# Kernel tuning notes

Hardware: AMD Instinct MI355X
Metric: run time of the kernel (lower is better)

The kernel has to match this reference:

```python
import jax, jax.numpy as jnp
import numpy as np

N = 100_000      # nodes
E = 3_200_000    # edges (avg degree 32)
D_IN = 128
D_H = 128
EPS = 1e-12      # F.normalize eps


def setup_inputs() -> dict:
    key = jax.random.key(0)
    k1, k2, k3 = jax.random.split(key, 3)
    X = jax.random.normal(k1, (N, D_IN), dtype=jnp.float32)
    edge_index = jax.random.randint(k2, (2, E), 0, N, dtype=jnp.int32)
    # GCNConv linear weight (stored as [in, out] for X @ W) and bias
    W = jax.random.normal(k3, (D_IN, D_H), dtype=jnp.float32) / np.sqrt(D_IN)
    b = jnp.zeros((D_H,), dtype=jnp.float32)
    # MessageNorm learnable scale, init 1.0
    scale = jnp.ones((1,), dtype=jnp.float32)
    return {"X": X, "edge_index": edge_index, "W": W, "b": b, "scale": scale}


def reference(X, edge_index, W, b, scale):
    n = X.shape[0]
    loop = jnp.arange(n, dtype=edge_index.dtype)
    src = jnp.concatenate([edge_index[0], loop])  # add self loops
    tgt = jnp.concatenate([edge_index[1], loop])
    # symmetric GCN normalization: D^{-1/2} (A+I) D^{-1/2}
    deg = jax.ops.segment_sum(jnp.ones_like(src, X.dtype), tgt, num_segments=n)
    dinv = jnp.where(deg > 0, jax.lax.rsqrt(deg), 0.0)
    norm = dinv[src] * dinv[tgt]  # [E+N]
    XW = X @ W  # [N, D_H]
    msg = jax.ops.segment_sum(norm[:, None] * XW[src], tgt, num_segments=n) + b
    # MessageNorm(learn_scale=True): l2-normalize msg, rescale by ||x||_2 * scale
    msg_n = msg / jnp.maximum(jnp.linalg.norm(msg, axis=-1, keepdims=True), EPS)
    x_norm = jnp.linalg.norm(X, axis=-1, keepdims=True)
    return jax.nn.gelu(msg_n * x_norm * scale, approximate=False)
```

## Files before the change

kernel.cpp:

```cpp
#include <hip/hip_runtime.h>
#include <math.h>

#define D 128
#define NB 391
#define BSH 8
#define BMASK 255
#define CAP 10240
#define EPB 4096
#define LDA 136

typedef unsigned short ushort_t;
typedef unsigned int uint_t;
typedef __attribute__((ext_vector_type(8))) short bfrag;
typedef __attribute__((ext_vector_type(4))) float ffrag;

__device__ inline ushort_t f2bf(float f) {
    uint_t u = __float_as_uint(f);
    uint_t r = (u + 0x7FFFu + ((u >> 16) & 1u)) >> 16;
    return (ushort_t)r;
}

__global__ __launch_bounds__(256) void k_bin(const int* __restrict__ src,
                                             const int* __restrict__ tgt, int e,
                                             int* __restrict__ bucket_cur,
                                             uint_t* __restrict__ binned,
                                             const float* __restrict__ W,
                                             ushort_t* __restrict__ Wt) {
    __shared__ int lcnt[NB];
    __shared__ int lbase[NB];
    int tid = threadIdx.x;

    if (blockIdx.x < 16) {
        int nrow = blockIdx.x * 8 + (tid >> 5);
        int k0 = (tid & 31) * 4;
        ushort4 o;
        o.x = f2bf(W[(size_t)(k0 + 0) * D + nrow]);
        o.y = f2bf(W[(size_t)(k0 + 1) * D + nrow]);
        o.z = f2bf(W[(size_t)(k0 + 2) * D + nrow]);
        o.w = f2bf(W[(size_t)(k0 + 3) * D + nrow]);
        *(ushort4*)&Wt[(size_t)nrow * D + k0] = o;
    }

    int base = blockIdx.x * EPB;
    for (int i = tid; i < NB; i += 256) lcnt[i] = 0;
    __syncthreads();

    int myb[16], myrank[16];
    uint_t myval[16];
#pragma unroll
    for (int k = 0; k < 16; ++k) {
        int i = base + k * 256 + tid;
        if (i < e) {
            int t = tgt[i];
            int s = src[i];
            int b = t >> BSH;
            myb[k] = b;
            myval[k] = ((uint_t)s << BSH) | (uint_t)(t & BMASK);
            myrank[k] = atomicAdd(&lcnt[b], 1);
        } else {
            myb[k] = -1;
        }
    }
    __syncthreads();
    for (int i = tid; i < NB; i += 256) {
        int c = lcnt[i];
        lbase[i] = (c > 0) ? atomicAdd(&bucket_cur[i], c) : 0;
    }
    __syncthreads();
#pragma unroll
    for (int k = 0; k < 16; ++k) {
        if (myb[k] >= 0) {
            int slot = lbase[myb[k]] + myrank[k];
            if (slot < CAP) binned[(size_t)myb[k] * CAP + slot] = myval[k];
        }
    }
}

__global__ __launch_bounds__(256) void k_sort(const uint_t* __restrict__ binned,
                                              const int* __restrict__ bucket_cur,
                                              int* __restrict__ col,
                                              int* __restrict__ rowptr,
                                              float* __restrict__ dinv, int n) {
    __shared__ uint_t sout[CAP];
    __shared__ int scnt[256];
    __shared__ int sincl[256];
    __shared__ int sofs[256];
    __shared__ int sred[256];
    int b = blockIdx.x;
    int tid = threadIdx.x;

    int v = 0;
    for (int i = tid; i < b; i += 256) v += min(bucket_cur[i], CAP);
    sred[tid] = v;
    __syncthreads();
    for (int off = 128; off >= 1; off >>= 1) {
        if (tid < off) sred[tid] += sred[tid + off];
        __syncthreads();
    }
    int baseg = sred[0];

    int nb = min(bucket_cur[b], CAP);
    const uint_t* bin = binned + (size_t)b * CAP;

    scnt[tid] = 0;
    __syncthreads();
    for (int i = tid; i < nb; i += 256)
        atomicAdd(&scnt[bin[i] & BMASK], 1);
    __syncthreads();
    int x = scnt[tid];
    sincl[tid] = x;
    __syncthreads();
    for (int off = 1; off < 256; off <<= 1) {
        int y = (tid >= off) ? sincl[tid - off] : 0;
        __syncthreads();
        x += y;
        sincl[tid] = x;
        __syncthreads();
    }
    sofs[tid] = x - scnt[tid];
    int t = (b << BSH) + tid;
    if (t < n) {
        rowptr[t + 1] = baseg + x;
        dinv[t] = rsqrtf((float)scnt[tid] + 1.0f);
    }
    if (b == 0 && tid == 0) rowptr[0] = 0;
    __syncthreads();
    for (int i = tid; i < nb; i += 256) {
        uint_t w = bin[i];
        int r = atomicAdd(&sofs[w & BMASK], 1);
        sout[r] = w >> BSH;
    }
    __syncthreads();
    for (int i = tid; i < nb; i += 256)
        col[baseg + i] = (int)sout[i];
}

__global__ __launch_bounds__(256) void k_gemm(const float* __restrict__ X,
                                              const ushort_t* __restrict__ Wt,
                                              const float* __restrict__ dinv,
                                              ushort_t* __restrict__ Y,
                                              float* __restrict__ xnorm, int n) {
    __shared__ ushort_t As[64 * LDA];
    __shared__ ushort_t Bs[128 * LDA];
    int tid = threadIdx.x;
    int row0 = blockIdx.x * 64;

    for (int i = tid; i < 128 * 16; i += 256) {
        int nr = i >> 4, c = (i & 15) << 3;
        *(uint4*)&Bs[nr * LDA + c] = *(const uint4*)&Wt[(size_t)nr * D + c];
    }

    const float4* X4 = (const float4*)X;
#pragma unroll
    for (int i2 = 0; i2 < 8; ++i2) {
        int item = i2 * 256 + tid;
        int r = item >> 5, c4 = item & 31;
        int gr = row0 + r;
        float4 v = (gr < n) ? X4[(size_t)gr * 32 + c4] : make_float4(0.f, 0.f, 0.f, 0.f);
        ushort4 bv;
        bv.x = f2bf(v.x); bv.y = f2bf(v.y); bv.z = f2bf(v.z); bv.w = f2bf(v.w);
        *(ushort4*)&As[r * LDA + c4 * 4] = bv;
        float s = v.x * v.x + v.y * v.y + v.z * v.z + v.w * v.w;
        s += __shfl_xor(s, 1);
        s += __shfl_xor(s, 2);
        s += __shfl_xor(s, 4);
        s += __shfl_xor(s, 8);
        s += __shfl_xor(s, 16);
        if ((tid & 31) == 0 && gr < n) xnorm[gr] = sqrtf(s);
    }
    __syncthreads();

    int w = tid >> 6;
    int lane = tid & 63;
    int q = lane >> 4;
    int mi = lane & 15;

    bfrag xf[4];
#pragma unroll
    for (int kt = 0; kt < 4; ++kt)
        xf[kt] = *(const bfrag*)&As[(w * 16 + mi) * LDA + kt * 32 + q * 8];

    ffrag acc[8];
#pragma unroll
    for (int nt = 0; nt < 8; ++nt) acc[nt] = (ffrag){0.f, 0.f, 0.f, 0.f};

#pragma unroll
    for (int nt = 0; nt < 8; ++nt) {
#pragma unroll
        for (int kt = 0; kt < 4; ++kt) {
            bfrag wf = *(const bfrag*)&Bs[(nt * 16 + mi) * LDA + kt * 32 + q * 8];
            acc[nt] = __builtin_amdgcn_mfma_f32_16x16x32_bf16(wf, xf[kt], acc[nt], 0, 0, 0);
        }
    }

    int gr = row0 + w * 16 + mi;
    if (gr < n) {
        float dv = dinv[gr];
#pragma unroll
        for (int nt = 0; nt < 8; ++nt) {
            ushort4 o;
            o.x = f2bf(acc[nt][0] * dv);
            o.y = f2bf(acc[nt][1] * dv);
            o.z = f2bf(acc[nt][2] * dv);
            o.w = f2bf(acc[nt][3] * dv);
            *(ushort4*)&Y[(size_t)gr * D + nt * 16 + q * 4] = o;
        }
    }
}

__global__ __launch_bounds__(256) void k_agg(const ushort_t* __restrict__ Y,
                                             const float* __restrict__ xnorm,
                                             const float* __restrict__ dinv,
                                             const int* __restrict__ rowptr,
                                             const int* __restrict__ col,
                                             const float* __restrict__ bias,
                                             const float* __restrict__ scale,
                                             float* __restrict__ out, int n) {
    int t = (blockIdx.x * 256 + threadIdx.x) >> 6;
    int lane = threadIdx.x & 63;
    if (t >= n) return;

    const char* Yb = (const char*)Y;
    uint_t lo4 = (uint_t)lane * 4;

    uint_t p = *(const uint_t*)(Yb + (((uint_t)t << 8) + lo4));
    float a0 = __uint_as_float(p << 16);
    float a1 = __uint_as_float(p & 0xFFFF0000u);

    int beg = rowptr[t];
    int end = rowptr[t + 1];
    int e = beg;
    for (; e + 16 <= end; e += 16) {
        uint_t qv[16];
#pragma unroll
        for (int k = 0; k < 16; ++k) {
            int s = col[e + k];
            qv[k] = *(const uint_t*)(Yb + (((uint_t)s << 8) + lo4));
        }
#pragma unroll
        for (int k = 0; k < 16; ++k) {
            a0 += __uint_as_float(qv[k] << 16);
            a1 += __uint_as_float(qv[k] & 0xFFFF0000u);
        }
    }
    for (; e + 4 <= end; e += 4) {
        uint_t qv[4];
#pragma unroll
        for (int k = 0; k < 4; ++k) {
            int s = col[e + k];
            qv[k] = *(const uint_t*)(Yb + (((uint_t)s << 8) + lo4));
        }
#pragma unroll
        for (int k = 0; k < 4; ++k) {
            a0 += __uint_as_float(qv[k] << 16);
            a1 += __uint_as_float(qv[k] & 0xFFFF0000u);
        }
    }
    for (; e < end; ++e) {
        int s = col[e];
        uint_t q = *(const uint_t*)(Yb + (((uint_t)s << 8) + lo4));
        a0 += __uint_as_float(q << 16);
        a1 += __uint_as_float(q & 0xFFFF0000u);
    }

    float dt = dinv[t];
    float m0 = fmaf(dt, a0, bias[lane * 2]);
    float m1 = fmaf(dt, a1, bias[lane * 2 + 1]);

    float m2 = m0 * m0 + m1 * m1;
#pragma unroll
    for (int m = 32; m >= 1; m >>= 1) m2 += __shfl_xor(m2, m);

    float denom = fmaxf(sqrtf(m2), 1e-12f);
    float fac = xnorm[t] * scale[0] / denom;
    float g0 = m0 * fac;
    float g1 = m1 * fac;
    float2 o;
    o.x = 0.5f * g0 * (1.0f + erff(g0 * 0.70710678118654752440f));
    o.y = 0.5f * g1 * (1.0f + erff(g1 * 0.70710678118654752440f));
    *(float2*)&out[(size_t)t * D + lane * 2] = o;
}


extern "C" void kernel_launch(void* const* d_in, const int* in_sizes, int n_in,
                              void* d_out, int out_size, void* d_ws, size_t ws_size,
                              hipStream_t stream) {
    const float* X     = (const float*)d_in[0];
    const int*   ei    = (const int*)d_in[1];
    const float* W     = (const float*)d_in[2];
    const float* bias  = (const float*)d_in[3];
    const float* scale = (const float*)d_in[4];
    float* out = (float*)d_out;

    int n = in_sizes[0] / D;
    int e = in_sizes[1] / 2;
    const int* src = ei;
    const int* tgt = ei + e;

    char* ws = (char*)d_ws;
    ushort_t* Y = (ushort_t*)ws;   ws += (size_t)n * D * sizeof(ushort_t);
    uint_t* binned = (uint_t*)Y;
    float* dinv = (float*)ws;      ws += (size_t)n * sizeof(float);
    float* xnorm = (float*)ws;     ws += (size_t)n * sizeof(float);
    int* rowptr = (int*)ws;        ws += (size_t)(n + 1) * sizeof(int);
    int* bucket_cur = (int*)ws;    ws += NB * sizeof(int);
    int* col = (int*)ws;           ws += (size_t)e * sizeof(int);
    ushort_t* Wt = (ushort_t*)ws;

    hipMemsetAsync(bucket_cur, 0, NB * sizeof(int), stream);
    k_bin<<<(e + EPB - 1) / EPB, 256, 0, stream>>>(src, tgt, e, bucket_cur, binned, W, Wt);
    k_sort<<<NB, 256, 0, stream>>>(binned, bucket_cur, col, rowptr, dinv, n);
    k_gemm<<<(n + 63) / 64, 256, 0, stream>>>(X, Wt, dinv, Y, xnorm, n);
    k_agg<<<(n + 3) / 4, 256, 0, stream>>>(Y, xnorm, dinv, rowptr, col, bias, scale, out, n);
}
```

Before: 315.1 us.

## Replace bucketed bin-sort CSR build with degree count, scan, and atomic scatter

Replaces the two-pass bucket-binning and per-bucket shared-memory sort with a classic CSR build: global atomic degree histogram, a three-kernel prefix scan, then a per-edge atomic scatter into col. This removes the intermediate binned buffer and the CAP truncation limit, but relies on millions of global atomics to random addresses and adds extra kernel launches. The neighbour order inside each row becomes nondeterministic and no longer sorted, which may hurt locality in the aggregation gathers.

Result: slower. 670.4 us (+112.8%).

```diff
diff --git a/kernel.cpp b/kernel.cpp
--- a/kernel.cpp
+++ b/kernel.cpp
@@ -2,12 +2,8 @@
 #include <math.h>
 
 #define D 128
-#define NB 391
-#define BSH 8
-#define BMASK 255
-#define CAP 10240
-#define EPB 4096
 #define LDA 136
+#define EPT_BLK 2048
 
 typedef unsigned short ushort_t;
 typedef unsigned int uint_t;
@@ -20,14 +16,10 @@
     return (ushort_t)r;
 }
 
-__global__ __launch_bounds__(256) void k_bin(const int* __restrict__ src,
-                                             const int* __restrict__ tgt, int e,
-                                             int* __restrict__ bucket_cur,
-                                             uint_t* __restrict__ binned,
+__global__ __launch_bounds__(256) void k_deg(const int* __restrict__ tgt, int e,
+                                             int* __restrict__ deg,
                                              const float* __restrict__ W,
                                              ushort_t* __restrict__ Wt) {
-    __shared__ int lcnt[NB];
-    __shared__ int lbase[NB];
     int tid = threadIdx.x;
 
     if (blockIdx.x < 16) {
@@ -41,98 +33,87 @@
         *(ushort4*)&Wt[(size_t)nrow * D + k0] = o;
     }
 
-    int base = blockIdx.x * EPB;
-    for (int i = tid; i < NB; i += 256) lcnt[i] = 0;
+    int base = blockIdx.x * EPT_BLK;
+#pragma unroll
+    for (int k = 0; k < 8; ++k) {
+        int i = base + k * 256 + tid;
+        if (i < e) atomicAdd(&deg[tgt[i]], 1);
+    }
+}
+
+__global__ __launch_bounds__(256) void k_scan1(const int* __restrict__ deg,
+                                               int* __restrict__ rowptr,
+                                               float* __restrict__ dinv,
+                                               int* __restrict__ bsum, int n) {
+    __shared__ int s[256];
+    int tid = threadIdx.x;
+    int i = blockIdx.x * 256 + tid;
+    int d = (i < n) ? deg[i] : 0;
+    int x = d;
+    s[tid] = x;
     __syncthreads();
-
-    int myb[16], myrank[16];
-    uint_t myval[16];
-#pragma unroll
-    for (int k = 0; k < 16; ++k) {
+    for (int off = 1; off < 256; off <<= 1) {
+        int y = (tid >= off) ? s[tid - off] : 0;
+        __syncthreads();
+        x += y;
+        s[tid] = x;
+        __syncthreads();
+    }
+    if (i < n) {
+        rowptr[i + 1] = x;
+        dinv[i] = rsqrtf((float)d + 1.0f);
+    }
+    if (tid == 255) bsum[blockIdx.x] = x;
+}
+
+__global__ __launch_bounds__(512) void k_scan2(int* __restrict__ bsum, int nb) {
+    __shared__ int s[512];
+    int tid = threadIdx.x;
+    int v = (tid < nb) ? bsum[tid] : 0;
+    int x = v;
+    s[tid] = x;
+    __syncthreads();
+    for (int off = 1; off < 512; off <<= 1) {
+        int y = (tid >= off) ? s[tid - off] : 0;
+        __syncthreads();
+        x += y;
+        s[tid] = x;
+        __syncthreads();
+    }
+    if (tid < nb) bsum[tid] = x - v;
+}
+
+__global__ __launch_bounds__(256) void k_scan3(const int* __restrict__ deg,
+                                               int* __restrict__ rowptr,
+                                               int* __restrict__ cur,
+                                               const int* __restrict__ bsum, int n) {
+    int tid = threadIdx.x;
+    int i = blockIdx.x * 256 + tid;
+    int off = bsum[blockIdx.x];
+    if (i < n) {
+        int v = rowptr[i + 1] + off;
+        rowptr[i + 1] = v;
+        cur[i] = v - deg[i];
+    }
+    if (i == 0) rowptr[0] = 0;
+}
+
+__global__ __launch_bounds__(256) void k_scatter(const int* __restrict__ src,
+                                                 const int* __restrict__ tgt, int e,
+                                                 int* __restrict__ cur,
+                                                 int* __restrict__ col) {
+    int tid = threadIdx.x;
+    int base = blockIdx.x * EPT_BLK;
+#pragma unroll
+    for (int k = 0; k < 8; ++k) {
         int i = base + k * 256 + tid;
         if (i < e) {
             int t = tgt[i];
             int s = src[i];
-            int b = t >> BSH;
-            myb[k] = b;
-            myval[k] = ((uint_t)s << BSH) | (uint_t)(t & BMASK);
-            myrank[k] = atomicAdd(&lcnt[b], 1);
-        } else {
-            myb[k] = -1;
-        }
-    }
-    __syncthreads();
-    for (int i = tid; i < NB; i += 256) {
-        int c = lcnt[i];
-        lbase[i] = (c > 0) ? atomicAdd(&bucket_cur[i], c) : 0;
-    }
-    __syncthreads();
-#pragma unroll
-    for (int k = 0; k < 16; ++k) {
-        if (myb[k] >= 0) {
-            int slot = lbase[myb[k]] + myrank[k];
-            if (slot < CAP) binned[(size_t)myb[k] * CAP + slot] = myval[k];
-        }
-    }
-}
-
-__global__ __launch_bounds__(256) void k_sort(const uint_t* __restrict__ binned,
-                                              const int* __restrict__ bucket_cur,
-                                              int* __restrict__ col,
-                                              int* __restrict__ rowptr,
-                                              float* __restrict__ dinv, int n) {
-    __shared__ uint_t sout[CAP];
-    __shared__ int scnt[256];
-    __shared__ int sincl[256];
-    __shared__ int sofs[256];
-    __shared__ int sred[256];
-    int b = blockIdx.x;
-    int tid = threadIdx.x;
-
-    int v = 0;
-    for (int i = tid; i < b; i += 256) v += min(bucket_cur[i], CAP);
-    sred[tid] = v;
-    __syncthreads();
-    for (int off = 128; off >= 1; off >>= 1) {
-        if (tid < off) sred[tid] += sred[tid + off];
-        __syncthreads();
-    }
-    int baseg = sred[0];
-
-    int nb = min(bucket_cur[b], CAP);
-    const uint_t* bin = binned + (size_t)b * CAP;
-
-    scnt[tid] = 0;
-    __syncthreads();
-    for (int i = tid; i < nb; i += 256)
-        atomicAdd(&scnt[bin[i] & BMASK], 1);
-    __syncthreads();
-    int x = scnt[tid];
-    sincl[tid] = x;
-    __syncthreads();
-    for (int off = 1; off < 256; off <<= 1) {
-        int y = (tid >= off) ? sincl[tid - off] : 0;
-        __syncthreads();
-        x += y;
-        sincl[tid] = x;
-        __syncthreads();
-    }
-    sofs[tid] = x - scnt[tid];
-    int t = (b << BSH) + tid;
-    if (t < n) {
-        rowptr[t + 1] = baseg + x;
-        dinv[t] = rsqrtf((float)scnt[tid] + 1.0f);
-    }
-    if (b == 0 && tid == 0) rowptr[0] = 0;
-    __syncthreads();
-    for (int i = tid; i < nb; i += 256) {
-        uint_t w = bin[i];
-        int r = atomicAdd(&sofs[w & BMASK], 1);
-        sout[r] = w >> BSH;
-    }
-    __syncthreads();
-    for (int i = tid; i < nb; i += 256)
-        col[baseg + i] = (int)sout[i];
+            int p = atomicAdd(&cur[t], 1);
+            col[p] = s;
+        }
+    }
 }
 
 __global__ __launch_bounds__(256) void k_gemm(const float* __restrict__ X,
@@ -299,17 +280,24 @@
 
     char* ws = (char*)d_ws;
     ushort_t* Y = (ushort_t*)ws;   ws += (size_t)n * D * sizeof(ushort_t);
-    uint_t* binned = (uint_t*)Y;
     float* dinv = (float*)ws;      ws += (size_t)n * sizeof(float);
     float* xnorm = (float*)ws;     ws += (size_t)n * sizeof(float);
     int* rowptr = (int*)ws;        ws += (size_t)(n + 1) * sizeof(int);
-    int* bucket_cur = (int*)ws;    ws += NB * sizeof(int);
+    int* deg = (int*)ws;           ws += (size_t)n * sizeof(int);
+    int* cur = (int*)ws;           ws += (size_t)n * sizeof(int);
+    int* bsum = (int*)ws;          ws += 512 * sizeof(int);
     int* col = (int*)ws;           ws += (size_t)e * sizeof(int);
     ushort_t* Wt = (ushort_t*)ws;
 
-    hipMemsetAsync(bucket_cur, 0, NB * sizeof(int), stream);
-    k_bin<<<(e + EPB - 1) / EPB, 256, 0, stream>>>(src, tgt, e, bucket_cur, binned, W, Wt);
-    k_sort<<<NB, 256, 0, stream>>>(binned, bucket_cur, col, rowptr, dinv, n);
+    int nscan = (n + 255) / 256;
+    int nedge = (e + EPT_BLK - 1) / EPT_BLK;
+
+    hipMemsetAsync(deg, 0, (size_t)n * sizeof(int), stream);
+    k_deg<<<nedge, 256, 0, stream>>>(tgt, e, deg, W, Wt);
+    k_scan1<<<nscan, 256, 0, stream>>>(deg, rowptr, dinv, bsum, n);
+    k_scan2<<<1, 512, 0, stream>>>(bsum, nscan);
+    k_scan3<<<nscan, 256, 0, stream>>>(deg, rowptr, cur, bsum, n);
+    k_scatter<<<nedge, 256, 0, stream>>>(src, tgt, e, cur, col);
     k_gemm<<<(n + 63) / 64, 256, 0, stream>>>(X, Wt, dinv, Y, xnorm, n);
     k_agg<<<(n + 3) / 4, 256, 0, stream>>>(Y, xnorm, dinv, rowptr, col, bias, scale, out, n);
 }
```
